# Performance work log

Measured on AMD Instinct MI355X. Metric: run time of the kernel, lower is better.

## Reference

```python
import jax, jax.numpy as jnp
import numpy as np

WS = 14  # window size
NH = 12  # num heads
EPS = 1e-5  # torch LayerNorm eps


def _rel_idx(ws: int) -> np.ndarray:
    coords = np.stack(np.meshgrid(np.arange(ws), np.arange(ws), indexing='ij'))
    cf = coords.reshape(2, -1)                      # (2, N)
    rel = cf[:, :, None] - cf[:, None, :]           # (2, N, N)
    rel = rel.transpose(1, 2, 0).copy()
    rel[:, :, 0] += ws - 1
    rel[:, :, 1] += ws - 1
    rel[:, :, 0] *= 2 * ws - 1
    return rel.sum(-1)                              # (N, N) int


def _layernorm(x, w, b):
    mu = jnp.mean(x, axis=-1, keepdims=True)
    var = jnp.var(x, axis=-1, keepdims=True)
    return (x - mu) * jax.lax.rsqrt(var + EPS) * w + b


def setup_inputs() -> dict:
    key = jax.random.key(0)
    ks = jax.random.split(key, 8)
    d, dff = 768, 3072
    s = lambda k, shape, sc: jax.random.normal(k, shape, jnp.float32) * sc
    return {
        'x': jax.random.normal(ks[0], (8, d, 56, 56), jnp.float32),
        'norm1_w': jnp.ones((d,), jnp.float32),
        'norm1_b': jnp.zeros((d,), jnp.float32),
        'qkv_w': s(ks[1], (d, 3 * d), 0.02),
        'qkv_b': jnp.zeros((3 * d,), jnp.float32),
        'rel_bias_table': s(ks[2], ((2 * WS - 1) ** 2, NH), 0.02),
        'proj_w': s(ks[3], (d, d), 0.02),
        'proj_b': jnp.zeros((d,), jnp.float32),
        'norm2_w': jnp.ones((d,), jnp.float32),
        'norm2_b': jnp.zeros((d,), jnp.float32),
        'fc1_w': s(ks[4], (d, dff), 0.02),
        'fc1_b': jnp.zeros((dff,), jnp.float32),
        'fc2_w': s(ks[5], (dff, d), 0.02),
        'fc2_b': jnp.zeros((d,), jnp.float32),
        'gamma1': jnp.full((d,), 1e-5, jnp.float32),
        'gamma2': jnp.full((d,), 1e-5, jnp.float32),
    }


def reference(x, norm1_w, norm1_b, qkv_w, qkv_b, rel_bias_table, proj_w, proj_b,
              norm2_w, norm2_b, fc1_w, fc1_b, fc2_w, fc2_b, gamma1, gamma2):
    B, C, H, W = x.shape
    nh, hd = NH, C // NH
    N = WS * WS
    xs = jnp.transpose(x, (0, 2, 3, 1))             # B,H,W,C
    shortcut = xs
    h = _layernorm(xs, norm1_w, norm1_b)

    # window partition (H, W divisible by WS)
    hw = h.reshape(B, H // WS, WS, W // WS, WS, C)
    hw = jnp.transpose(hw, (0, 1, 3, 2, 4, 5)).reshape(-1, N, C)  # (Bw, N, C)

    qkv = hw @ qkv_w + qkv_b                        # (Bw, N, 3C)
    qkv = qkv.reshape(-1, N, 3, nh, hd)
    q, k, v = [jnp.transpose(qkv[:, :, i], (0, 2, 1, 3)) for i in range(3)]  # (Bw,nh,N,hd)

    attn = jnp.einsum('bhnd,bhmd->bhnm', q, k) * (hd ** -0.5)
    rel_idx = jnp.asarray(_rel_idx(WS))             # static (N,N)
    bias = rel_bias_table[rel_idx]                  # (N,N,nh)
    attn = attn + jnp.transpose(bias, (2, 0, 1))[None]
    attn = jax.nn.softmax(attn, axis=-1)

    out = jnp.einsum('bhnm,bhmd->bnhd', attn, v).reshape(-1, N, C)
    out = out @ proj_w + proj_b                     # (Bw, N, C)

    # window reverse
    out = out.reshape(B, H // WS, W // WS, WS, WS, C)
    out = jnp.transpose(out, (0, 1, 3, 2, 4, 5)).reshape(B, H, W, C)

    xs = shortcut + gamma1 * out
    h2 = _layernorm(xs, norm2_w, norm2_b)
    mlp = jax.nn.gelu(h2 @ fc1_w + fc1_b, approximate=False) @ fc2_w + fc2_b
    xs = xs + gamma2 * mlp
    return jnp.transpose(xs, (0, 3, 1, 2))          # B,C,H,W
```

## Files before the change

### kernel.cpp

```cpp
#include <hip/hip_runtime.h>
#include <cstdint>
#include <cstddef>


typedef unsigned short u16;
typedef short short8 __attribute__((ext_vector_type(8)));
typedef float floatx4 __attribute__((ext_vector_type(4)));

static __device__ __forceinline__ float bf2f(u16 u) {
  return __uint_as_float(((unsigned)u) << 16);
}
static __device__ __forceinline__ u16 f2bf(float f) {
  unsigned u = __float_as_uint(f);
  return (u16)((u + 0x7FFFu + ((u >> 16) & 1u)) >> 16);
}
static __device__ __forceinline__ float ldin(const void* p, size_t i, int isf) {
  return isf ? ((const float*)p)[i] : bf2f(((const u16*)p)[i]);
}
static __device__ __forceinline__ void gload_lds16(const void* g, void* l) {
  __builtin_amdgcn_global_load_lds(
      (const __attribute__((address_space(1))) void*)g,
      (__attribute__((address_space(3))) void*)l, 16, 0, 0);
}

__global__ __launch_bounds__(256) void detect_kernel(const u16* __restrict__ x,
                                                     int* __restrict__ flag) {
  __shared__ int tot;
  if (threadIdx.x == 0) tot = 0;
  __syncthreads();
  int cnt = 0;
  for (int i = threadIdx.x; i < 4096; i += 256) {
    int e = (x[i] >> 7) & 0xFF;
    if (e >= 0xC1) cnt++;
  }
  atomicAdd(&tot, cnt);
  __syncthreads();
  if (threadIdx.x == 0) flag[0] = (tot > 16) ? 1 : 0;
}

__global__ __launch_bounds__(256) void cvt_params_kernel(
    const void* n1w, const void* n1b, const void* qkvb, const void* projb,
    const void* n2w, const void* n2b, const void* fc1b, const void* fc2b,
    const void* g1, const void* g2, const void* bt, u16* __restrict__ P,
    const int* __restrict__ flag) {
  int isf = *flag;
  int i = blockIdx.x * 256 + threadIdx.x;
  const void* src; int off;
  if      (i < 768)   { src = n1w;   off = i; }
  else if (i < 1536)  { src = n1b;   off = i - 768; }
  else if (i < 3840)  { src = qkvb;  off = i - 1536; }
  else if (i < 4608)  { src = projb; off = i - 3840; }
  else if (i < 5376)  { src = n2w;   off = i - 4608; }
  else if (i < 6144)  { src = n2b;   off = i - 5376; }
  else if (i < 9216)  { src = fc1b;  off = i - 6144; }
  else if (i < 9984)  { src = fc2b;  off = i - 9216; }
  else if (i < 10752) { src = g1;    off = i - 9984; }
  else if (i < 11520) { src = g2;    off = i - 10752; }
  else if (i < 20268) { src = bt;    off = i - 11520; }
  else return;
  P[i] = f2bf(ldin(src, off, isf));
}

__global__ __launch_bounds__(256) void wtr_kernel(const void* __restrict__ W,
                                                  u16* __restrict__ WT,
                                                  int K, int N,
                                                  const int* __restrict__ flag) {
  int isf = *flag;
  __shared__ u16 tl[32][33];
  int tx = threadIdx.x, ty = threadIdx.y;
  int n0 = blockIdx.x * 32, k0 = blockIdx.y * 32;
#pragma unroll
  for (int j = 0; j < 32; j += 8)
    tl[ty + j][tx] = f2bf(ldin(W, (size_t)(k0 + ty + j) * N + n0 + tx, isf));
  __syncthreads();
#pragma unroll
  for (int j = 0; j < 32; j += 8)
    WT[(size_t)(n0 + ty + j) * K + k0 + tx] = tl[tx][ty + j];
}

__global__ __launch_bounds__(256) void tin_kernel(const void* __restrict__ x,
                                                  u16* __restrict__ sc,
                                                  const int* __restrict__ flag) {
  int isf = *flag;
  int cc = blockIdx.x, h = blockIdx.y, b = blockIdx.z;
  __shared__ u16 tile[64 * 57];
  int tid = threadIdx.x;
  for (int i = tid; i < 64 * 56; i += 256) {
    int ci = i / 56, w = i - ci * 56;
    tile[ci * 57 + w] =
        f2bf(ldin(x, (((size_t)b * 768 + cc * 64 + ci) * 56 + h) * 56 + w, isf));
  }
  __syncthreads();
  int hb = h / 14, hi = h - hb * 14;
  for (int i = tid; i < 56 * 64; i += 256) {
    int w = i >> 6, ci = i & 63;
    int wb = w / 14, wj = w - wb * 14;
    int r = (b * 16 + hb * 4 + wb) * 196 + hi * 14 + wj;
    sc[(size_t)r * 768 + cc * 64 + ci] = tile[ci * 57 + w];
  }
}

__global__ __launch_bounds__(256) void tout_kernel(const u16* __restrict__ src,
                                                   void* __restrict__ out,
                                                   const int* __restrict__ flag) {
  int isf = *flag;
  int cc = blockIdx.x, h = blockIdx.y, b = blockIdx.z;
  __shared__ u16 tile[64 * 57];
  int tid = threadIdx.x;
  int hb = h / 14, hi = h - hb * 14;
  for (int i = tid; i < 56 * 64; i += 256) {
    int w = i >> 6, ci = i & 63;
    int wb = w / 14, wj = w - wb * 14;
    int r = (b * 16 + hb * 4 + wb) * 196 + hi * 14 + wj;
    tile[ci * 57 + w] = src[(size_t)r * 768 + cc * 64 + ci];
  }
  __syncthreads();
  for (int i = tid; i < 64 * 56; i += 256) {
    int ci = i / 56, w = i - ci * 56;
    size_t o = (((size_t)b * 768 + cc * 64 + ci) * 56 + h) * 56 + w;
    if (isf) ((float*)out)[o] = bf2f(tile[ci * 57 + w]);
    else     ((u16*)out)[o]   = tile[ci * 57 + w];
  }
}

__global__ __launch_bounds__(256) void ln_kernel(const u16* __restrict__ xin,
                                                 const u16* __restrict__ wt,
                                                 const u16* __restrict__ bs,
                                                 u16* __restrict__ out) {
  int row = blockIdx.x, t = threadIdx.x;
  const u16* xr = xin + (size_t)row * 768;
  float v0 = bf2f(xr[t]), v1 = bf2f(xr[t + 256]), v2 = bf2f(xr[t + 512]);
  float s1 = v0 + v1 + v2;
  float s2 = v0 * v0 + v1 * v1 + v2 * v2;
#pragma unroll
  for (int off = 32; off > 0; off >>= 1) {
    s1 += __shfl_xor(s1, off);
    s2 += __shfl_xor(s2, off);
  }
  __shared__ float p1[4], p2[4];
  if ((t & 63) == 0) { p1[t >> 6] = s1; p2[t >> 6] = s2; }
  __syncthreads();
  float S1 = p1[0] + p1[1] + p1[2] + p1[3];
  float S2 = p2[0] + p2[1] + p2[2] + p2[3];
  float mu = S1 * (1.f / 768.f);
  float var = S2 * (1.f / 768.f) - mu * mu;
  float rs = rsqrtf(var + 1e-5f);
  u16* orow = out + (size_t)row * 768;
  orow[t]       = f2bf((v0 - mu) * rs * bf2f(wt[t])       + bf2f(bs[t]));
  orow[t + 256] = f2bf((v1 - mu) * rs * bf2f(wt[t + 256]) + bf2f(bs[t + 256]));
  orow[t + 512] = f2bf((v2 - mu) * rs * bf2f(wt[t + 512]) + bf2f(bs[t + 512]));
}

template <int EPI>
__global__ __launch_bounds__(256) void gemm_kernel(
    const u16* __restrict__ A, const u16* __restrict__ BT,
    const u16* __restrict__ bias, const u16* __restrict__ gamma,
    u16* out, int N, int K, int NX, int NY) {
  int bid = blockIdx.x;
  int r8 = bid & 7, q = bid >> 3;
  int xb = q % NX, yb = (q / NX) * 8 + r8;
  if (yb >= NY) return;

  __shared__ u16 As[128 * 32];
  __shared__ u16 Bs[128 * 32];
  int tid = threadIdx.x;
  int w = tid >> 6, l = tid & 63;
  int lane15 = l & 15, quad = l >> 4;
  int m0 = yb * 128, n0 = xb * 128;
  int wm = w & 1, wn = w >> 1;
  floatx4 acc[4][4];
#pragma unroll
  for (int i = 0; i < 4; i++)
#pragma unroll
    for (int j = 0; j < 4; j++)
#pragma unroll
      for (int e = 0; e < 4; e++) acc[i][j][e] = 0.f;

  const u16* Abase = A + (size_t)m0 * K;
  const u16* Bbase = BT + (size_t)n0 * K;
  int rseg = l >> 2, ch = l & 3;

  for (int kt = 0; kt < K; kt += 32) {
    __syncthreads();
#pragma unroll
    for (int sI = 0; sI < 2; ++sI) {
      int s = w * 2 + sI;
      gload_lds16(Abase + (size_t)(s * 16 + rseg) * K + kt + ch * 8, &As[s * 512]);
      gload_lds16(Bbase + (size_t)(s * 16 + rseg) * K + kt + ch * 8, &Bs[s * 512]);
    }
    __syncthreads();
    short8 af[4], bf[4];
#pragma unroll
    for (int mi = 0; mi < 4; ++mi)
      af[mi] = *(const short8*)&As[(wm * 64 + mi * 16 + lane15) * 32 + quad * 8];
#pragma unroll
    for (int ni = 0; ni < 4; ++ni)
      bf[ni] = *(const short8*)&Bs[(wn * 64 + ni * 16 + lane15) * 32 + quad * 8];
#pragma unroll
    for (int mi = 0; mi < 4; ++mi)
#pragma unroll
      for (int ni = 0; ni < 4; ++ni)
        acc[mi][ni] = __builtin_amdgcn_mfma_f32_16x16x32_bf16(
            af[mi], bf[ni], acc[mi][ni], 0, 0, 0);
  }

#pragma unroll
  for (int mi = 0; mi < 4; ++mi) {
    int row0 = m0 + wm * 64 + mi * 16 + quad * 4;
#pragma unroll
    for (int ni = 0; ni < 4; ++ni) {
      int col = n0 + wn * 64 + ni * 16 + lane15;
      float bv = bf2f(bias[col]);
#pragma unroll
      for (int reg = 0; reg < 4; ++reg) {
        int row = row0 + reg;
        float v = acc[mi][ni][reg] + bv;
        size_t idx = (size_t)row * N + col;
        if (EPI == 0) {
          out[idx] = f2bf(v);
        } else if (EPI == 1) {
          out[idx] = f2bf(bf2f(out[idx]) + bf2f(gamma[col]) * v);
        } else {
          out[idx] = f2bf(0.5f * v * (1.f + erff(v * 0.70710678118f)));
        }
      }
    }
  }
}

__global__ __launch_bounds__(256) void attn_kernel(const u16* __restrict__ qkv,
                                                   const u16* __restrict__ btab,
                                                   u16* __restrict__ out) {
  __shared__ __align__(16) u16 VT[64 * 232];
  __shared__ __align__(16) u16 Pa[4 * 2 * 512];
  __shared__ float bS[729];
  int bid = blockIdx.x;
  int win = bid / 12, h = bid - win * 12;
  int tid = threadIdx.x, w = tid >> 6, l = tid & 63;
  int lane15 = l & 15, quad = l >> 4;
  const u16* qbase = qkv + (size_t)win * 196 * 2304;

  for (int i = tid; i < 64 * 28; i += 256) {
    int d = i / 28, m = i - d * 28;
    VT[d * 232 + 196 + m] = 0;
  }
  for (int i = tid; i < 196 * 64; i += 256) {
    int m = i >> 6, d = i & 63;
    VT[d * 232 + m] = qbase[(size_t)m * 2304 + 1536 + h * 64 + d];
  }
  for (int i = tid; i < 729; i += 256) bS[i] = bf2f(btab[i * 12 + h]);
  __syncthreads();

  u16* Pw = Pa + w * 1024;
  for (int rt = w; rt < 13; rt += 4) {
    floatx4 acc[13];
#pragma unroll
    for (int nt = 0; nt < 13; ++nt)
#pragma unroll
      for (int e = 0; e < 4; ++e) acc[nt][e] = 0.f;

    int rq = rt * 16 + lane15;
    bool qok = rq < 196;
#pragma unroll
    for (int kk = 0; kk < 2; ++kk) {
      short8 qf;
      if (qok)
        qf = *(const short8*)&qbase[(size_t)rq * 2304 + h * 64 + kk * 32 + quad * 8];
      else
#pragma unroll
        for (int e = 0; e < 8; ++e) qf[e] = 0;
#pragma unroll
      for (int nt = 0; nt < 13; ++nt) {
        int n = nt * 16 + lane15;
        short8 kf = *(const short8*)&qbase[(size_t)n * 2304 + 768 + h * 64 + kk * 32 + quad * 8];
        acc[nt] = __builtin_amdgcn_mfma_f32_16x16x32_bf16(qf, kf, acc[nt], 0, 0, 0);
      }
    }

    int i1[4], j1[4]; bool rv[4]; float mx[4], sm[4];
#pragma unroll
    for (int reg = 0; reg < 4; ++reg) {
      int r = rt * 16 + quad * 4 + reg;
      i1[reg] = r / 14; j1[reg] = r - i1[reg] * 14;
      rv[reg] = r < 196; mx[reg] = -1e30f; sm[reg] = 0.f;
    }
#pragma unroll
    for (int nt = 0; nt < 13; ++nt) {
      int cc = nt * 16 + lane15;
      bool cv = cc < 196;
      int i2 = cc / 14, j2 = cc - i2 * 14;
#pragma unroll
      for (int reg = 0; reg < 4; ++reg) {
        float v;
        if (cv) {
          v = acc[nt][reg] * 0.125f;
          if (rv[reg]) v += bS[(i1[reg] - i2 + 13) * 27 + (j1[reg] - j2 + 13)];
        } else v = -1e30f;
        acc[nt][reg] = v;
        mx[reg] = fmaxf(mx[reg], v);
      }
    }
#pragma unroll
    for (int reg = 0; reg < 4; ++reg)
#pragma unroll
      for (int off = 1; off < 16; off <<= 1)
        mx[reg] = fmaxf(mx[reg], __shfl_xor(mx[reg], off));
#pragma unroll
    for (int nt = 0; nt < 13; ++nt)
#pragma unroll
      for (int reg = 0; reg < 4; ++reg) {
        float p = __expf(acc[nt][reg] - mx[reg]);
        acc[nt][reg] = p; sm[reg] += p;
      }
#pragma unroll
    for (int reg = 0; reg < 4; ++reg) {
#pragma unroll
      for (int off = 1; off < 16; off <<= 1) sm[reg] += __shfl_xor(sm[reg], off);
      sm[reg] = 1.f / sm[reg];
    }

    floatx4 oa[4];
#pragma unroll
    for (int dt = 0; dt < 4; ++dt)
#pragma unroll
      for (int e = 0; e < 4; ++e) oa[dt][e] = 0.f;
#pragma unroll
    for (int kk = 0; kk < 7; ++kk) {
      u16* Pb = Pw + (kk & 1) * 512;
#pragma unroll
      for (int p = 0; p < 2; ++p) {
        int nt = kk * 2 + p;
#pragma unroll
        for (int reg = 0; reg < 4; ++reg) {
          float v = (nt < 13) ? acc[nt][reg] * sm[reg] : 0.f;
          Pb[(quad * 4 + reg) * 32 + p * 16 + lane15] = f2bf(v);
        }
      }
      asm volatile("s_waitcnt lgkmcnt(0)" ::: "memory");
      short8 pf = *(const short8*)&Pb[lane15 * 32 + quad * 8];
#pragma unroll
      for (int dt = 0; dt < 4; ++dt) {
        short8 vf = *(const short8*)&VT[(dt * 16 + lane15) * 232 + kk * 32 + quad * 8];
        oa[dt] = __builtin_amdgcn_mfma_f32_16x16x32_bf16(pf, vf, oa[dt], 0, 0, 0);
      }
    }
#pragma unroll
    for (int dt = 0; dt < 4; ++dt)
#pragma unroll
      for (int reg = 0; reg < 4; ++reg) {
        int r = rt * 16 + quad * 4 + reg;
        if (r < 196)
          out[((size_t)win * 196 + r) * 768 + h * 64 + dt * 16 + lane15] =
              f2bf(oa[dt][reg]);
      }
  }
}

static inline int gemm_grid(int NX, int NY) { return NX * ((NY + 7) / 8) * 8; }

extern "C" void kernel_launch(void* const* d_in, const int* in_sizes, int n_in,
                              void* d_out, int out_size, void* d_ws, size_t ws_size,
                              hipStream_t stream) {
  const void* x      = d_in[0];
  const void* n1w    = d_in[1];
  const void* n1b    = d_in[2];
  const void* qkv_w  = d_in[3];
  const void* qkv_b  = d_in[4];
  const void* btab   = d_in[5];
  const void* proj_w = d_in[6];
  const void* proj_b = d_in[7];
  const void* n2w    = d_in[8];
  const void* n2b    = d_in[9];
  const void* fc1_w  = d_in[10];
  const void* fc1_b  = d_in[11];
  const void* fc2_w  = d_in[12];
  const void* fc2_b  = d_in[13];
  const void* gamma1 = d_in[14];
  const void* gamma2 = d_in[15];
  (void)in_sizes; (void)n_in; (void)out_size;

  int c;
  if      (ws_size >= 245432576ull) c = 1;
  else if (ws_size >= 168362240ull) c = 2;
  else                              c = 4;
  const int R = 25088 / c;
  const int WN = 128 / c;
  const int NY = R / 128;

  char* ws = (char*)d_ws;
  int*  flag  = (int*)ws;
  u16*  P     = (u16*)(ws + 256);
  u16*  qkvT  = (u16*)(ws + 65792);
  u16*  projT = (u16*)(ws + 65792 + 3538944);
  u16*  fc1T  = (u16*)(ws + 65792 + 4718592);
  u16*  fc2T  = (u16*)(ws + 65792 + 9437184);
  const size_t B0 = 38535168;
  u16*  buf0  = (u16*)(ws + 14221568);
  u16*  buf1  = (u16*)(ws + 14221568 + B0);
  char* scr   = ws + 14221568 + 2 * B0;

  u16 *p_n1w = P, *p_n1b = P + 768, *p_qkvb = P + 1536, *p_projb = P + 3840;
  u16 *p_n2w = P + 4608, *p_n2b = P + 5376, *p_fc1b = P + 6144;
  u16 *p_fc2b = P + 9216, *p_g1 = P + 9984, *p_g2 = P + 10752, *p_bt = P + 11520;

  dim3 b256(256), bw(32, 8);
  detect_kernel<<<dim3(1), b256, 0, stream>>>((const u16*)x, flag);
  cvt_params_kernel<<<dim3(80), b256, 0, stream>>>(
      n1w, n1b, qkv_b, proj_b, n2w, n2b, fc1_b, fc2_b, gamma1, gamma2, btab,
      P, flag);
  wtr_kernel<<<dim3(72, 24), bw, 0, stream>>>(qkv_w, qkvT, 768, 2304, flag);
  wtr_kernel<<<dim3(24, 24), bw, 0, stream>>>(proj_w, projT, 768, 768, flag);
  wtr_kernel<<<dim3(96, 24), bw, 0, stream>>>(fc1_w, fc1T, 768, 3072, flag);
  wtr_kernel<<<dim3(24, 96), bw, 0, stream>>>(fc2_w, fc2T, 3072, 768, flag);

  tin_kernel<<<dim3(12, 56, 8), b256, 0, stream>>>(x, buf0, flag);
  ln_kernel<<<dim3(25088), b256, 0, stream>>>(buf0, p_n1w, p_n1b, buf1);

  for (int hc = 0; hc < c; ++hc) {
    size_t ro = (size_t)hc * R * 768;
    u16* qC = (u16*)scr;
    u16* aC = (u16*)(scr + (size_t)R * 4608);
    gemm_kernel<0><<<dim3(gemm_grid(18, NY)), b256, 0, stream>>>(
        buf1 + ro, qkvT, p_qkvb, nullptr, qC, 2304, 768, 18, NY);
    attn_kernel<<<dim3(WN * 12), b256, 0, stream>>>(qC, p_bt, aC);
    gemm_kernel<1><<<dim3(gemm_grid(6, NY)), b256, 0, stream>>>(
        aC, projT, p_projb, p_g1, buf0 + ro, 768, 768, 6, NY);
  }

  ln_kernel<<<dim3(25088), b256, 0, stream>>>(buf0, p_n2w, p_n2b, buf1);

  for (int hc = 0; hc < c; ++hc) {
    size_t ro = (size_t)hc * R * 768;
    u16* gC = (u16*)scr;
    gemm_kernel<2><<<dim3(gemm_grid(24, NY)), b256, 0, stream>>>(
        buf1 + ro, fc1T, p_fc1b, nullptr, gC, 3072, 768, 24, NY);
    gemm_kernel<1><<<dim3(gemm_grid(6, NY)), b256, 0, stream>>>(
        gC, fc2T, p_fc2b, p_g2, buf0 + ro, 768, 3072, 6, NY);
  }

  tout_kernel<<<dim3(12, 56, 8), b256, 0, stream>>>(buf0, d_out, flag);
}
```

Measured before the change: 1.051 ms.

## Stage GEMM epilogue through LDS for vectorized stores and use fast GELU

For the plain and GELU GEMM epilogues, results are written into a shared-memory tile and then stored to global memory as 16-byte rows, replacing scattered 2-byte stores. The exact erf GELU is replaced with a tanh-style sigmoid approximation using __expf. This targets store inefficiency and the cost of erff in the fc1 epilogue, at the price of extra LDS (about 34KB), two barriers and small numerical deviation from exact GELU.

```diff
diff --git a/kernel.cpp b/kernel.cpp
--- a/kernel.cpp
+++ b/kernel.cpp
@@ -21,6 +21,10 @@
   __builtin_amdgcn_global_load_lds(
       (const __attribute__((address_space(1))) void*)g,
       (__attribute__((address_space(3))) void*)l, 16, 0, 0);
+}
+static __device__ __forceinline__ float fast_gelu(float v) {
+  float u2 = v * (1.5957691216f + 0.0713548163f * v * v);
+  return v * (1.0f / (1.0f + __expf(-u2)));
 }
 
 __global__ __launch_bounds__(256) void detect_kernel(const u16* __restrict__ x,
@@ -204,26 +208,48 @@
             af[mi], bf[ni], acc[mi][ni], 0, 0, 0);
   }
 
-#pragma unroll
-  for (int mi = 0; mi < 4; ++mi) {
-    int row0 = m0 + wm * 64 + mi * 16 + quad * 4;
-#pragma unroll
-    for (int ni = 0; ni < 4; ++ni) {
-      int col = n0 + wn * 64 + ni * 16 + lane15;
-      float bv = bf2f(bias[col]);
-#pragma unroll
-      for (int reg = 0; reg < 4; ++reg) {
-        int row = row0 + reg;
-        float v = acc[mi][ni][reg] + bv;
-        size_t idx = (size_t)row * N + col;
-        if (EPI == 0) {
-          out[idx] = f2bf(v);
-        } else if (EPI == 1) {
-          out[idx] = f2bf(bf2f(out[idx]) + bf2f(gamma[col]) * v);
-        } else {
-          out[idx] = f2bf(0.5f * v * (1.f + erff(v * 0.70710678118f)));
+  if constexpr (EPI == 1) {
+#pragma unroll
+    for (int mi = 0; mi < 4; ++mi) {
+      int row0 = m0 + wm * 64 + mi * 16 + quad * 4;
+#pragma unroll
+      for (int ni = 0; ni < 4; ++ni) {
+        int col = n0 + wn * 64 + ni * 16 + lane15;
+        float bv = bf2f(bias[col]);
+        float gv = bf2f(gamma[col]);
+#pragma unroll
+        for (int reg = 0; reg < 4; ++reg) {
+          size_t idx = (size_t)(row0 + reg) * N + col;
+          float v = acc[mi][ni][reg] + bv;
+          out[idx] = f2bf(bf2f(out[idx]) + gv * v);
         }
       }
+    }
+  } else {
+    __shared__ __align__(16) u16 Cs[128 * 136];
+    __syncthreads();
+#pragma unroll
+    for (int mi = 0; mi < 4; ++mi) {
+      int rl0 = wm * 64 + mi * 16 + quad * 4;
+#pragma unroll
+      for (int ni = 0; ni < 4; ++ni) {
+        int cl = wn * 64 + ni * 16 + lane15;
+        float bv = bf2f(bias[n0 + cl]);
+#pragma unroll
+        for (int reg = 0; reg < 4; ++reg) {
+          float v = acc[mi][ni][reg] + bv;
+          if (EPI == 2) v = fast_gelu(v);
+          Cs[(rl0 + reg) * 136 + cl] = f2bf(v);
+        }
+      }
+    }
+    __syncthreads();
+    int rr = tid >> 4, cc8 = (tid & 15) * 8;
+#pragma unroll
+    for (int chk = 0; chk < 8; ++chk) {
+      int row = chk * 16 + rr;
+      short8 val = *(const short8*)&Cs[row * 136 + cc8];
+      *(short8*)(out + (size_t)(m0 + row) * N + n0 + cc8) = val;
     }
   }
 }
```

Result: no change. 1.049 ms (-0.2%).
